# Kernel optimization log

Measured on AMD Instinct MI355X. Metric: run time of the kernel, lower is better.

Reference implementation:

```python
import jax, jax.numpy as jnp
import numpy as np

B, T, D = 2, 2048, 2048
H, KVH = 32, 8
HD = D // H            # 64
G = H // KVH           # 4


def setup_inputs() -> dict:
    key = jax.random.key(0)
    k1, k2, k3 = jax.random.split(key, 3)
    x_q = jax.random.normal(k1, (B, T, D), dtype=jnp.float32)
    W_qkv = jax.random.normal(k2, (D, H * HD + 2 * KVH * HD), dtype=jnp.float32) * 0.02
    W_out = jax.random.normal(k3, (D, D), dtype=jnp.float32) * 0.02
    b_out = jnp.zeros((D,), dtype=jnp.float32)
    # real rotary tables: theta = 10000^{-2i/HD}
    inv_freq = 1.0 / (10000.0 ** (np.arange(0, HD, 2) / HD))   # [HD/2]
    pos = np.arange(T)[:, None] * inv_freq[None, :]            # [T, HD/2]
    rope_cos = jnp.asarray(np.cos(pos), dtype=jnp.float32)
    rope_sin = jnp.asarray(np.sin(pos), dtype=jnp.float32)
    return {"x_q": x_q, "W_qkv": W_qkv, "W_out": W_out, "b_out": b_out,
            "rope_cos": rope_cos, "rope_sin": rope_sin}


def _apply_rope(x, cos, sin):
    # x: [B, h, T, HD], cos/sin: [T, HD/2] -> interleaved even/odd rotation
    xe = x[..., 0::2]
    xo = x[..., 1::2]
    c = cos[None, None, :, :]
    s = sin[None, None, :, :]
    return jnp.stack([xe * c - xo * s, xe * s + xo * c], axis=-1).reshape(x.shape)


def reference(x_q, W_qkv, W_out, b_out, rope_cos, rope_sin):
    b, t, d = x_q.shape
    qkv = x_q @ W_qkv                                  # [B,T,3072]
    q_lin = qkv[..., : H * HD]
    k_lin = qkv[..., H * HD: H * HD + KVH * HD]
    v_lin = qkv[..., H * HD + KVH * HD:]
    q = q_lin.reshape(b, t, H, HD).transpose(0, 2, 1, 3)        # [B,H,T,HD]
    k = k_lin.reshape(b, t, KVH, HD).transpose(0, 2, 1, 3)      # [B,KVH,T,HD]
    v = v_lin.reshape(b, t, KVH, HD).transpose(0, 2, 1, 3)
    # GQA expand (repeat_interleave over heads)
    k = jnp.repeat(k, G, axis=1)                                # [B,H,T,HD]
    v = jnp.repeat(v, G, axis=1)
    q = _apply_rope(q, rope_cos[:t], rope_sin[:t])
    k = _apply_rope(k, rope_cos[:t], rope_sin[:t])
    scale = 1.0 / jnp.sqrt(jnp.asarray(HD, dtype=x_q.dtype))
    logits = jnp.einsum('bhqd,bhkd->bhqk', q, k) * scale        # [B,H,T,T]
    causal = jnp.triu(jnp.ones((t, t), dtype=bool), 1)[None, None]
    logits = jnp.where(causal, jnp.finfo(logits.dtype).min, logits)
    attn = jax.nn.softmax(logits, axis=-1)
    out = jnp.einsum('bhqk,bhkd->bhqd', attn, v)                # [B,H,T,HD]
    out = out.transpose(0, 2, 1, 3).reshape(b, t, H * HD)       # [B,T,D]
    out = out @ W_out + b_out
    return jnp.nan_to_num(out, nan=0.0, posinf=1e4, neginf=-1e4)
```

## Files before the change

### kernel.cpp

```cpp
#include <hip/hip_runtime.h>
#include <hip/hip_bf16.h>

#define DI __device__ __forceinline__

#if __has_builtin(__builtin_amdgcn_exp2f)
#define EXP2(x) __builtin_amdgcn_exp2f(x)
#else
#define EXP2(x) exp2f(x)
#endif

namespace {

constexpr int Bc = 2, Tc = 2048, Dc = 2048, Hc = 32, KVHc = 8, HDc = 64;
constexpr int NQKV = Hc * HDc + 2 * KVHc * HDc;

typedef __bf16 bf16x8 __attribute__((ext_vector_type(8)));
typedef unsigned short u16x8 __attribute__((ext_vector_type(8)));
typedef unsigned short u16x4 __attribute__((ext_vector_type(4)));
typedef float f32x4 __attribute__((ext_vector_type(4)));

union FragU { u16x8 u; bf16x8 b; u16x4 h[2]; };

DI float bits2f(unsigned int u) {
  union { unsigned int i; float f; } v; v.i = u << 16; return v.f;
}
DI unsigned short f2bits(float f) {
  __hip_bfloat16 h = __float2bfloat16(f);
  return *reinterpret_cast<unsigned short*>(&h);
}

DI void store_out(float* p, float v) { *p = v; }
DI void store_out(__hip_bfloat16* p, float v) { *p = __float2bfloat16(v); }

typedef __attribute__((address_space(1))) void gv_t;
typedef __attribute__((address_space(3))) void lv_t;

template<int ROWB, int TOTB, bool SWZ = false>
DI void stage_tile(const char* g, long long row_stride_b, char* lds) {
  const int tid = threadIdx.x;
  const int wid = tid >> 6, lane = tid & 63;
#pragma unroll
  for (int it = 0; it < TOTB / 4096; ++it) {
    int off = it * 4096 + wid * 1024 + lane * 16;
    int row = off / ROWB;
    int colb = off % ROWB;
    if (SWZ) colb ^= (row & 7) << 4;
    const char* gp = g + (long long)row * row_stride_b + colb;
    char* lp = lds + it * 4096 + wid * 1024;
    __builtin_amdgcn_global_load_lds((gv_t*)gp, (lv_t*)lp, 16, 0, 0);
  }
}

__global__ __launch_bounds__(256) void cvt_f32_bf16(
    const float* __restrict__ in, __hip_bfloat16* __restrict__ out) {
  const long long i = ((long long)blockIdx.x * 256 + threadIdx.x) * 8;
  const float4 a = *(const float4*)(in + i);
  const float4 b = *(const float4*)(in + i + 4);
  u16x8 r;
  r[0] = f2bits(a.x); r[1] = f2bits(a.y); r[2] = f2bits(a.z); r[3] = f2bits(a.w);
  r[4] = f2bits(b.x); r[5] = f2bits(b.y); r[6] = f2bits(b.z); r[7] = f2bits(b.w);
  *(u16x8*)((unsigned short*)out + i) = r;
}

__global__ __launch_bounds__(256) void transpose_cvt_kernel(
    const float* __restrict__ in, __hip_bfloat16* __restrict__ out, int R, int C) {
  __shared__ unsigned short tile[64][65];
  const int c0 = blockIdx.x * 64, r0 = blockIdx.y * 64;
  const int tid = threadIdx.x;
  const int rr = tid >> 2, seg = (tid & 3) * 16;
  const float* src = in + (long long)(r0 + rr) * C + c0 + seg;
#pragma unroll
  for (int i = 0; i < 16; ++i) tile[rr][seg + i] = f2bits(src[i]);
  __syncthreads();
  unsigned short* dst = (unsigned short*)out + (long long)(c0 + rr) * R + r0 + seg;
#pragma unroll
  for (int i = 0; i < 16; ++i) dst[i] = tile[seg + i][rr];
}

__global__ __launch_bounds__(256) void transpose_kernel(
    const __hip_bfloat16* __restrict__ in, __hip_bfloat16* __restrict__ out,
    int R, int C) {
  __shared__ unsigned short tile[64][65];
  const long long slice = (long long)R * C;
  const unsigned short* ip = (const unsigned short*)in + (long long)blockIdx.z * slice;
  unsigned short* op = (unsigned short*)out + (long long)blockIdx.z * slice;
  const int c0 = blockIdx.x * 64, r0 = blockIdx.y * 64;
  const int tid = threadIdx.x;
  const int rr = tid >> 2, seg = (tid & 3) * 16;
  const unsigned short* src = ip + (long long)(r0 + rr) * C + c0 + seg;
#pragma unroll
  for (int i = 0; i < 16; ++i) tile[rr][seg + i] = src[i];
  __syncthreads();
  unsigned short* dst = op + (long long)(c0 + rr) * R + r0 + seg;
#pragma unroll
  for (int i = 0; i < 16; ++i) dst[i] = tile[seg + i][rr];
}

template <typename OT>
__global__ __launch_bounds__(256) void gemm_bt(
    const __hip_bfloat16* __restrict__ A, const __hip_bfloat16* __restrict__ Bt,
    const float* __restrict__ bias, OT* __restrict__ C, int M, int N, int K) {
  __shared__ __align__(16) char As[2][8192];
  __shared__ __align__(16) char Bs[2][8192];
  const int nwgx = N >> 7;
  const int nwg = nwgx * (M >> 7);
  const int bid0 = blockIdx.y * nwgx + blockIdx.x;
  const int cpx = nwg >> 3;
  const int bid = (bid0 & 7) * cpx + (bid0 >> 3);
  const int n0 = (bid % nwgx) * 128;
  const int m0 = (bid / nwgx) * 128;
  const int tid = threadIdx.x;
  const int wid = tid >> 6, lane = tid & 63;
  const int wm = (wid >> 1) * 64, wn = (wid & 1) * 64;
  const int l15 = lane & 15, quad = lane >> 4;

  const char* Ag = (const char*)(A + (long long)m0 * K);
  const char* Bg = (const char*)(Bt + (long long)n0 * K);
  const long long strb = (long long)K * 2;

  f32x4 acc[4][4] = {};
  const int nk = K >> 5;

  stage_tile<64, 8192>(Ag, strb, As[0]);
  stage_tile<64, 8192>(Bg, strb, Bs[0]);
  stage_tile<64, 8192>(Ag + 64, strb, As[1]);
  stage_tile<64, 8192>(Bg + 64, strb, Bs[1]);

  for (int kt = 0; kt < nk; ++kt) {
    if (kt < nk - 1) asm volatile("s_waitcnt vmcnt(4)" ::: "memory");
    else             asm volatile("s_waitcnt vmcnt(0)" ::: "memory");
    __builtin_amdgcn_sched_barrier(0);
    __builtin_amdgcn_s_barrier();
    __builtin_amdgcn_sched_barrier(0);

    const char* as = As[kt & 1];
    const char* bs = Bs[kt & 1];
    FragU a[4], b[4];
#pragma unroll
    for (int mt = 0; mt < 4; ++mt)
      a[mt].u = *(const u16x8*)(as + ((wm + mt * 16 + l15) * 32 + quad * 8) * 2);
#pragma unroll
    for (int nt = 0; nt < 4; ++nt)
      b[nt].u = *(const u16x8*)(bs + ((wn + nt * 16 + l15) * 32 + quad * 8) * 2);
#pragma unroll
    for (int mt = 0; mt < 4; ++mt)
#pragma unroll
      for (int nt = 0; nt < 4; ++nt)
        acc[mt][nt] =
            __builtin_amdgcn_mfma_f32_16x16x32_bf16(a[mt].b, b[nt].b, acc[mt][nt], 0, 0, 0);

    __builtin_amdgcn_sched_barrier(0);
    __builtin_amdgcn_s_barrier();
    __builtin_amdgcn_sched_barrier(0);
    if (kt + 2 < nk) {
      stage_tile<64, 8192>(Ag + (long long)(kt + 2) * 64, strb, As[kt & 1]);
      stage_tile<64, 8192>(Bg + (long long)(kt + 2) * 64, strb, Bs[kt & 1]);
    }
  }

#pragma unroll
  for (int nt = 0; nt < 4; ++nt) {
    const int col = n0 + wn + nt * 16 + l15;
    const float bv = bias ? bias[col] : 0.f;
#pragma unroll
    for (int mt = 0; mt < 4; ++mt) {
#pragma unroll
      for (int r = 0; r < 4; ++r) {
        const int row = m0 + wm + mt * 16 + quad * 4 + r;
        store_out(C + (long long)row * N + col, acc[mt][nt][r] + bv);
      }
    }
  }
}

__global__ __launch_bounds__(384) void rope_reshape(
    const __hip_bfloat16* __restrict__ qkv, const float* __restrict__ cosb,
    const float* __restrict__ sinb, __hip_bfloat16* __restrict__ Qo,
    __hip_bfloat16* __restrict__ Ko, __hip_bfloat16* __restrict__ Vo) {
  constexpr float SCL = 0.125f * 1.44269504088896f;
  const int row = blockIdx.x;
  const int b = row / Tc, t = row % Tc;
  const unsigned short* src = (const unsigned short*)qkv + (long long)row * NQKV;
  const float* cb = cosb + t * 32;
  const float* sb = sinb + t * 32;
  const int e = (int)threadIdx.x * 8;
  const u16x8 v = *(const u16x8*)(src + e);
  if (e < Hc * HDc) {
    const int hh = e >> 6, d = e & 63, ii = d >> 1;
    u16x8 r;
#pragma unroll
    for (int p = 0; p < 4; ++p) {
      const float c = cb[ii + p], s = sb[ii + p];
      const float xe = bits2f(v[2 * p]), xo = bits2f(v[2 * p + 1]);
      r[2 * p] = f2bits((xe * c - xo * s) * SCL);
      r[2 * p + 1] = f2bits((xe * s + xo * c) * SCL);
    }
    const long long idx = (((long long)b * Hc + hh) * Tc + t) * HDc + d;
    *(u16x8*)((unsigned short*)Qo + idx) = r;
  } else if (e < Hc * HDc + KVHc * HDc) {
    const int e2 = e - Hc * HDc;
    const int kh = e2 >> 6, d = e2 & 63, ii = d >> 1;
    u16x8 r;
#pragma unroll
    for (int p = 0; p < 4; ++p) {
      const float c = cb[ii + p], s = sb[ii + p];
      const float xe = bits2f(v[2 * p]), xo = bits2f(v[2 * p + 1]);
      r[2 * p] = f2bits(xe * c - xo * s);
      r[2 * p + 1] = f2bits(xe * s + xo * c);
    }
    const long long idx = (((long long)b * KVHc + kh) * Tc + t) * HDc + d;
    *(u16x8*)((unsigned short*)Ko + idx) = r;
  } else {
    const int e2 = e - (Hc * HDc + KVHc * HDc);
    const int kh = e2 >> 6, d = e2 & 63;
    const long long idx = (((long long)b * KVHc + kh) * Tc + t) * HDc + d;
    *(u16x8*)((unsigned short*)Vo + idx) = v;
  }
}


DI void mask_diag(f32x4 (&S)[4], int wid, int l15, int quad) {
#pragma unroll
  for (int nt = 0; nt < 4; ++nt)
#pragma unroll
    for (int r = 0; r < 4; ++r)
      if ((nt * 16 + quad * 4 + r) > (wid * 16 + l15)) S[nt][r] = -1e30f;
}

DI float softmax_pack(f32x4 (&S)[4], float& m_i, float& l_i, FragU (&pa)[2]) {
  float mx = fmaxf(fmaxf(S[0][0], S[0][1]), fmaxf(S[0][2], S[0][3]));
#pragma unroll
  for (int nt = 1; nt < 4; ++nt)
    mx = fmaxf(mx, fmaxf(fmaxf(S[nt][0], S[nt][1]), fmaxf(S[nt][2], S[nt][3])));
  mx = fmaxf(mx, __shfl_xor(mx, 16, 64));
  mx = fmaxf(mx, __shfl_xor(mx, 32, 64));
  const float mnew = fmaxf(m_i, mx);
  const float alpha = EXP2(m_i - mnew);
  m_i = mnew;
  float sum = 0.f;
#pragma unroll
  for (int nt = 0; nt < 4; ++nt)
#pragma unroll
    for (int r = 0; r < 4; ++r) {
      const float pp = EXP2(S[nt][r] - mnew);
      S[nt][r] = pp;
      sum += pp;
    }
  sum += __shfl_xor(sum, 16, 64);
  sum += __shfl_xor(sum, 32, 64);
  l_i = l_i * alpha + sum;
#pragma unroll
  for (int ks = 0; ks < 2; ++ks)
#pragma unroll
    for (int r = 0; r < 4; ++r) {
      pa[ks].u[r] = f2bits(S[2 * ks][r]);
      pa[ks].u[4 + r] = f2bits(S[2 * ks + 1][r]);
    }
  return alpha;
}

DI void attn_tile(const char* __restrict__ Ksb, const char* __restrict__ Vsb,
                  const FragU (&qa)[2], f32x4 (&O)[4], float& m_i, float& l_i,
                  bool diag, int wid, int l15, int quad, int sw) {
  f32x4 S[4] = {};
  __builtin_amdgcn_s_setprio(1);
#pragma unroll
  for (int nt = 0; nt < 4; ++nt) {
#pragma unroll
    for (int ks = 0; ks < 2; ++ks) {
      FragU kb;
      kb.u = *(const u16x8*)(Ksb + (nt * 16 + l15) * 128 + ((((ks << 2) | quad) ^ sw) << 4));
      S[nt] = __builtin_amdgcn_mfma_f32_16x16x32_bf16(kb.b, qa[ks].b, S[nt], 0, 0, 0);
    }
  }
  __builtin_amdgcn_s_setprio(0);
  if (diag) mask_diag(S, wid, l15, quad);
  FragU pa[2];
  const float alpha = softmax_pack(S, m_i, l_i, pa);
#pragma unroll
  for (int nt = 0; nt < 4; ++nt)
#pragma unroll
    for (int r = 0; r < 4; ++r) O[nt][r] *= alpha;
  __builtin_amdgcn_s_setprio(1);
#pragma unroll
  for (int nt = 0; nt < 4; ++nt) {
    const char* vrow = Vsb + (nt * 16 + l15) * 128 + ((quad & 1) << 3);
    const int gq = quad >> 1;
#pragma unroll
    for (int ks = 0; ks < 2; ++ks) {
      FragU vb;
      vb.h[0] = *(const u16x4*)(vrow + (((ks * 4 + gq) ^ sw) << 4));
      vb.h[1] = *(const u16x4*)(vrow + (((ks * 4 + gq + 2) ^ sw) << 4));
      O[nt] = __builtin_amdgcn_mfma_f32_16x16x32_bf16(vb.b, pa[ks].b, O[nt], 0, 0, 0);
    }
  }
  __builtin_amdgcn_s_setprio(0);
}

DI void attn_tile_dual(const char* __restrict__ Ksb, const char* __restrict__ Vsb,
                       const FragU (&qaB)[2], const FragU (&qaA)[2],
                       f32x4 (&OB)[4], f32x4 (&OA)[4],
                       float& mB, float& lB, float& mA, float& lA,
                       bool diagA, int wid, int l15, int quad, int sw) {
  f32x4 SB[4] = {}, SA[4] = {};
  __builtin_amdgcn_s_setprio(1);
#pragma unroll
  for (int nt = 0; nt < 4; ++nt) {
#pragma unroll
    for (int ks = 0; ks < 2; ++ks) {
      FragU kb;
      kb.u = *(const u16x8*)(Ksb + (nt * 16 + l15) * 128 + ((((ks << 2) | quad) ^ sw) << 4));
      SB[nt] = __builtin_amdgcn_mfma_f32_16x16x32_bf16(kb.b, qaB[ks].b, SB[nt], 0, 0, 0);
      SA[nt] = __builtin_amdgcn_mfma_f32_16x16x32_bf16(kb.b, qaA[ks].b, SA[nt], 0, 0, 0);
    }
  }
  __builtin_amdgcn_s_setprio(0);
  if (diagA) mask_diag(SA, wid, l15, quad);
  FragU paB[2], paA[2];
  const float aB = softmax_pack(SB, mB, lB, paB);
  const float aA = softmax_pack(SA, mA, lA, paA);
#pragma unroll
  for (int nt = 0; nt < 4; ++nt)
#pragma unroll
    for (int r = 0; r < 4; ++r) {
      OB[nt][r] *= aB;
      OA[nt][r] *= aA;
    }
  __builtin_amdgcn_s_setprio(1);
#pragma unroll
  for (int nt = 0; nt < 4; ++nt) {
    const char* vrow = Vsb + (nt * 16 + l15) * 128 + ((quad & 1) << 3);
    const int gq = quad >> 1;
#pragma unroll
    for (int ks = 0; ks < 2; ++ks) {
      FragU vb;
      vb.h[0] = *(const u16x4*)(vrow + (((ks * 4 + gq) ^ sw) << 4));
      vb.h[1] = *(const u16x4*)(vrow + (((ks * 4 + gq + 2) ^ sw) << 4));
      OB[nt] = __builtin_amdgcn_mfma_f32_16x16x32_bf16(vb.b, paB[ks].b, OB[nt], 0, 0, 0);
      OA[nt] = __builtin_amdgcn_mfma_f32_16x16x32_bf16(vb.b, paA[ks].b, OA[nt], 0, 0, 0);
    }
  }
  __builtin_amdgcn_s_setprio(0);
}

__global__ __launch_bounds__(256, 4) void attn_kernel(
    const __hip_bfloat16* __restrict__ Q, const __hip_bfloat16* __restrict__ K,
    const __hip_bfloat16* __restrict__ Vt, __hip_bfloat16* __restrict__ Out) {
  __shared__ __align__(16) char Ks[2][8192];
  __shared__ __align__(16) char Vs[2][8192];

  const int p = blockIdx.x;
  const int qtA = p, qtB = (Tc / 64 - 1) - p;
  const int h = blockIdx.y, b = blockIdx.z;
  const int kvh = h >> 2;
  const int tid = threadIdx.x, wid = tid >> 6, lane = tid & 63;
  const int l15 = lane & 15, quad = lane >> 4;
  const int sw = l15 & 7;

  const char* QgA = (const char*)(Q + (((long long)b * Hc + h) * Tc + qtA * 64) * HDc);
  const char* QgB = (const char*)(Q + (((long long)b * Hc + h) * Tc + qtB * 64) * HDc);
  const char* Kg = (const char*)(K + (((long long)b * KVHc + kvh) * Tc) * HDc);
  const char* Vg = (const char*)(Vt + (((long long)b * KVHc + kvh) * HDc) * Tc);

  FragU qaA[2], qaB[2];
#pragma unroll
  for (int ks = 0; ks < 2; ++ks) {
    const int qoff = (wid * 16 + l15) * 128 + (((ks << 2) | quad) << 4);
    qaA[ks].u = *(const u16x8*)(QgA + qoff);
    qaB[ks].u = *(const u16x8*)(QgB + qoff);
  }

  f32x4 OA[4] = {}, OB[4] = {};
  float mA = -1e30f, lA = 0.f, mB = -1e30f, lB = 0.f;

  stage_tile<128, 8192, true>(Kg, 128, Ks[0]);
  stage_tile<128, 8192, true>(Vg, (long long)Tc * 2, Vs[0]);
  asm volatile("s_waitcnt vmcnt(0)" ::: "memory");
  __syncthreads();

  for (int j = 0; j <= qtB; ++j) {
    const int cur = j & 1;
    if (j < qtB) {
      stage_tile<128, 8192, true>(Kg + (long long)(j + 1) * 8192, 128, Ks[cur ^ 1]);
      stage_tile<128, 8192, true>(Vg + (long long)(j + 1) * 128, (long long)Tc * 2, Vs[cur ^ 1]);
    }

    if (j <= qtA) {
      attn_tile_dual(Ks[cur], Vs[cur], qaB, qaA, OB, OA, mB, lB, mA, lA,
                     j == qtA, wid, l15, quad, sw);
    } else {
      attn_tile(Ks[cur], Vs[cur], qaB, OB, mB, lB, j == qtB, wid, l15, quad, sw);
    }

    asm volatile("s_waitcnt vmcnt(0)" ::: "memory");
    __syncthreads();
  }

  const float invA = 1.0f / lA, invB = 1.0f / lB;
  const int tA = qtA * 64 + wid * 16 + l15;
  const int tB = qtB * 64 + wid * 16 + l15;
  unsigned short* obA =
      (unsigned short*)Out + ((long long)b * Tc + tA) * Dc + h * 64 + quad * 4;
  unsigned short* obB =
      (unsigned short*)Out + ((long long)b * Tc + tB) * Dc + h * 64 + quad * 4;
#pragma unroll
  for (int nt = 0; nt < 4; ++nt) {
    u16x4 va, vb;
#pragma unroll
    for (int r = 0; r < 4; ++r) {
      va[r] = f2bits(OA[nt][r] * invA);
      vb[r] = f2bits(OB[nt][r] * invB);
    }
    *(u16x4*)(obA + nt * 16) = va;
    *(u16x4*)(obB + nt * 16) = vb;
  }
}

}

extern "C" void kernel_launch(void* const* d_in, const int* in_sizes, int n_in,
                              void* d_out, int out_size, void* d_ws, size_t ws_size,
                              hipStream_t stream) {
  const float* x_q  = (const float*)d_in[0];
  const float* Wqkv = (const float*)d_in[1];
  const float* Wout = (const float*)d_in[2];
  const float* bout = (const float*)d_in[3];
  const float* rc   = (const float*)d_in[4];
  const float* rs   = (const float*)d_in[5];
  float* out = (float*)d_out;

  constexpr size_t SZ_QKV   = (size_t)Bc * Tc * NQKV * 2;
  constexpr size_t SZ_XB    = (size_t)Bc * Tc * Dc * 2;
  constexpr size_t SZ_QB    = (size_t)Bc * Hc * Tc * HDc * 2;
  constexpr size_t SZ_KV    = (size_t)Bc * KVHc * Tc * HDc * 2;
  constexpr size_t SZ_AO    = (size_t)Bc * Tc * Dc * 2;
  constexpr size_t OFF_QKV   = 0;
  constexpr size_t OFF_XB    = SZ_QKV;
  constexpr size_t OFF_WQKVT = SZ_QKV + SZ_XB;
  constexpr size_t OFF_QB    = SZ_QKV;
  constexpr size_t OFF_KB    = OFF_QB + SZ_QB;
  constexpr size_t OFF_VTMP  = OFF_KB + SZ_KV;
  constexpr size_t OFF_VT    = 0;
  constexpr size_t OFF_AO    = SZ_KV;
  constexpr size_t OFF_WOUTT = OFF_AO + SZ_AO;

  char* w = (char*)d_ws;
  __hip_bfloat16* qkv   = (__hip_bfloat16*)(w + OFF_QKV);
  __hip_bfloat16* xb    = (__hip_bfloat16*)(w + OFF_XB);
  __hip_bfloat16* WqkvT = (__hip_bfloat16*)(w + OFF_WQKVT);
  __hip_bfloat16* Qb    = (__hip_bfloat16*)(w + OFF_QB);
  __hip_bfloat16* Kb    = (__hip_bfloat16*)(w + OFF_KB);
  __hip_bfloat16* Vtmp  = (__hip_bfloat16*)(w + OFF_VTMP);
  __hip_bfloat16* Vt    = (__hip_bfloat16*)(w + OFF_VT);
  __hip_bfloat16* AO    = (__hip_bfloat16*)(w + OFF_AO);
  __hip_bfloat16* WoutT = (__hip_bfloat16*)(w + OFF_WOUTT);

  cvt_f32_bf16<<<dim3((Bc * Tc * Dc) / (256 * 8)), 256, 0, stream>>>(x_q, xb);

  transpose_cvt_kernel<<<dim3(NQKV / 64, Dc / 64), 256, 0, stream>>>(Wqkv, WqkvT, Dc, NQKV);

  gemm_bt<__hip_bfloat16><<<dim3(NQKV / 128, (Bc * Tc) / 128), 256, 0, stream>>>(
      xb, WqkvT, nullptr, qkv, Bc * Tc, NQKV, Dc);

  rope_reshape<<<dim3(Bc * Tc), 384, 0, stream>>>(qkv, rc, rs, Qb, Kb, Vtmp);

  transpose_kernel<<<dim3(HDc / 64, Tc / 64, Bc * KVHc), 256, 0, stream>>>(Vtmp, Vt, Tc, HDc);

  attn_kernel<<<dim3(Tc / 128, Hc, Bc), 256, 0, stream>>>(Qb, Kb, Vt, AO);

  transpose_cvt_kernel<<<dim3(Dc / 64, Dc / 64), 256, 0, stream>>>(Wout, WoutT, Dc, Dc);

  gemm_bt<float><<<dim3(Dc / 128, (Bc * Tc) / 128), 256, 0, stream>>>(
      AO, WoutT, bout, out, Bc * Tc, Dc, Dc);
}
```

Before: 330.3 us.

## Rewrite GEMM as 256x128 tile with 512 threads and triple-buffered swizzled LDS

Replaces the 128x128, 256-thread GEMM with a 256x128 tile run by 8 waves, using a K-step of 64 and three LDS buffers with an XOR swizzle to avoid bank conflicts. Prefetch of the next tile is interleaved between the two K sub-steps, and MFMA sections get raised wave priority. The goal is more data reuse per tile and better overlap of global loads with MFMA work. The cost is heavy LDS use (144KB) that limits occupancy to one block per CU, and fewer workgroups in the grid.

```diff
diff --git a/kernel.cpp b/kernel.cpp
--- a/kernel.cpp
+++ b/kernel.cpp
@@ -47,6 +47,21 @@
     if (SWZ) colb ^= (row & 7) << 4;
     const char* gp = g + (long long)row * row_stride_b + colb;
     char* lp = lds + it * 4096 + wid * 1024;
+    __builtin_amdgcn_global_load_lds((gv_t*)gp, (lv_t*)lp, 16, 0, 0);
+  }
+}
+
+template<int TOTB>
+DI void stage512(const char* g, long long row_stride_b, char* lds) {
+  const int tid = threadIdx.x;
+  const int wid = tid >> 6, lane = tid & 63;
+#pragma unroll
+  for (int it = 0; it < TOTB / 8192; ++it) {
+    const int off = it * 8192 + wid * 1024 + lane * 16;
+    const int row = off >> 7;
+    const int colb = (off & 127) ^ ((row & 7) << 4);
+    const char* gp = g + (long long)row * row_stride_b + colb;
+    char* lp = lds + it * 8192 + wid * 1024;
     __builtin_amdgcn_global_load_lds((gv_t*)gp, (lv_t*)lp, 16, 0, 0);
   }
 }
@@ -97,65 +112,82 @@
 }
 
 template <typename OT>
-__global__ __launch_bounds__(256) void gemm_bt(
+__global__ __launch_bounds__(512, 1) void gemm256(
     const __hip_bfloat16* __restrict__ A, const __hip_bfloat16* __restrict__ Bt,
     const float* __restrict__ bias, OT* __restrict__ C, int M, int N, int K) {
-  __shared__ __align__(16) char As[2][8192];
-  __shared__ __align__(16) char Bs[2][8192];
+  __shared__ __align__(16) char As[3][32768];
+  __shared__ __align__(16) char Bs[3][16384];
   const int nwgx = N >> 7;
-  const int nwg = nwgx * (M >> 7);
+  const int nwg = nwgx * (M >> 8);
   const int bid0 = blockIdx.y * nwgx + blockIdx.x;
   const int cpx = nwg >> 3;
   const int bid = (bid0 & 7) * cpx + (bid0 >> 3);
   const int n0 = (bid % nwgx) * 128;
-  const int m0 = (bid / nwgx) * 128;
+  const int m0 = (bid / nwgx) * 256;
   const int tid = threadIdx.x;
   const int wid = tid >> 6, lane = tid & 63;
   const int wm = (wid >> 1) * 64, wn = (wid & 1) * 64;
   const int l15 = lane & 15, quad = lane >> 4;
+  const int sw = l15 & 7;
 
   const char* Ag = (const char*)(A + (long long)m0 * K);
   const char* Bg = (const char*)(Bt + (long long)n0 * K);
   const long long strb = (long long)K * 2;
+  const int nkt = K >> 6;
 
   f32x4 acc[4][4] = {};
-  const int nk = K >> 5;
-
-  stage_tile<64, 8192>(Ag, strb, As[0]);
-  stage_tile<64, 8192>(Bg, strb, Bs[0]);
-  stage_tile<64, 8192>(Ag + 64, strb, As[1]);
-  stage_tile<64, 8192>(Bg + 64, strb, Bs[1]);
-
-  for (int kt = 0; kt < nk; ++kt) {
-    if (kt < nk - 1) asm volatile("s_waitcnt vmcnt(4)" ::: "memory");
-    else             asm volatile("s_waitcnt vmcnt(0)" ::: "memory");
+
+  stage512<32768>(Ag, strb, As[0]);
+  stage512<16384>(Bg, strb, Bs[0]);
+  stage512<32768>(Ag + 128, strb, As[1]);
+  stage512<16384>(Bg + 128, strb, Bs[1]);
+
+  for (int kt = 0; kt < nkt; ++kt) {
+    if (kt + 1 < nkt) asm volatile("s_waitcnt vmcnt(6)" ::: "memory");
+    else              asm volatile("s_waitcnt vmcnt(0)" ::: "memory");
     __builtin_amdgcn_sched_barrier(0);
     __builtin_amdgcn_s_barrier();
     __builtin_amdgcn_sched_barrier(0);
 
-    const char* as = As[kt & 1];
-    const char* bs = Bs[kt & 1];
-    FragU a[4], b[4];
-#pragma unroll
-    for (int mt = 0; mt < 4; ++mt)
-      a[mt].u = *(const u16x8*)(as + ((wm + mt * 16 + l15) * 32 + quad * 8) * 2);
-#pragma unroll
-    for (int nt = 0; nt < 4; ++nt)
-      b[nt].u = *(const u16x8*)(bs + ((wn + nt * 16 + l15) * 32 + quad * 8) * 2);
-#pragma unroll
-    for (int mt = 0; mt < 4; ++mt)
+    const char* ab = As[kt % 3];
+    const char* bb = Bs[kt % 3];
+    const int pf = kt + 2;
+    const bool do_pf = pf < nkt;
+    char* pfA = As[pf % 3];
+    char* pfB = Bs[pf % 3];
+    const char* gA = Ag + (long long)pf * 128;
+    const char* gB = Bg + (long long)pf * 128;
+
+#pragma unroll
+    for (int kk = 0; kk < 2; ++kk) {
+      FragU a[4], b[4];
+#pragma unroll
+      for (int mt = 0; mt < 4; ++mt)
+        a[mt].u = *(const u16x8*)(ab + (wm + mt * 16 + l15) * 128 +
+                                  ((((kk << 2) | quad) ^ sw) << 4));
 #pragma unroll
       for (int nt = 0; nt < 4; ++nt)
-        acc[mt][nt] =
-            __builtin_amdgcn_mfma_f32_16x16x32_bf16(a[mt].b, b[nt].b, acc[mt][nt], 0, 0, 0);
-
+        b[nt].u = *(const u16x8*)(bb + (wn + nt * 16 + l15) * 128 +
+                                  ((((kk << 2) | quad) ^ sw) << 4));
+      if (do_pf) {
+        if (kk == 0) stage512<32768>(gA, strb, pfA);
+        else         stage512<16384>(gB, strb, pfB);
+      }
+      __builtin_amdgcn_sched_barrier(0);
+      asm volatile("s_waitcnt lgkmcnt(0)" ::: "memory");
+      __builtin_amdgcn_sched_barrier(0);
+      __builtin_amdgcn_s_setprio(1);
+#pragma unroll
+      for (int mt = 0; mt < 4; ++mt)
+#pragma unroll
+        for (int nt = 0; nt < 4; ++nt)
+          acc[mt][nt] =
+              __builtin_amdgcn_mfma_f32_16x16x32_bf16(a[mt].b, b[nt].b, acc[mt][nt], 0, 0, 0);
+      __builtin_amdgcn_s_setprio(0);
+    }
     __builtin_amdgcn_sched_barrier(0);
     __builtin_amdgcn_s_barrier();
     __builtin_amdgcn_sched_barrier(0);
-    if (kt + 2 < nk) {
-      stage_tile<64, 8192>(Ag + (long long)(kt + 2) * 64, strb, As[kt & 1]);
-      stage_tile<64, 8192>(Bg + (long long)(kt + 2) * 64, strb, Bs[kt & 1]);
-    }
   }
 
 #pragma unroll
@@ -459,7 +491,7 @@
 
   transpose_cvt_kernel<<<dim3(NQKV / 64, Dc / 64), 256, 0, stream>>>(Wqkv, WqkvT, Dc, NQKV);
 
-  gemm_bt<__hip_bfloat16><<<dim3(NQKV / 128, (Bc * Tc) / 128), 256, 0, stream>>>(
+  gemm256<__hip_bfloat16><<<dim3(NQKV / 128, (Bc * Tc) / 256), 512, 0, stream>>>(
       xb, WqkvT, nullptr, qkv, Bc * Tc, NQKV, Dc);
 
   rope_reshape<<<dim3(Bc * Tc), 384, 0, stream>>>(qkv, rc, rs, Qb, Kb, Vtmp);
@@ -470,6 +502,6 @@
 
   transpose_cvt_kernel<<<dim3(Dc / 64, Dc / 64), 256, 0, stream>>>(Wout, WoutT, Dc, Dc);
 
-  gemm_bt<float><<<dim3(Dc / 128, (Bc * Tc) / 128), 256, 0, stream>>>(
+  gemm256<float><<<dim3(Dc / 128, (Bc * Tc) / 256), 512, 0, stream>>>(
       AO, WoutT, bout, out, Bc * Tc, Dc, Dc);
 }
```

Result: no change. 332.1 us (+0.6%).

## Share staged K/V tiles across two wave groups per attention block

Applied to the files above, without the earlier changes.

The attention kernel grows to 512 threads, with two 4-wave groups each owning a pair of causal query tiles: (p, 31-p) and (15-p, 16+p). Both groups read the same K/V tiles staged once into LDS, which halves the global K/V traffic and staging work per query tile. A new stage512 helper spreads each 8KB tile load across 8 waves. The grid halves, so there are fewer blocks, and the group with less causal work sits idle at the shared barriers while the other group finishes.

```diff
diff --git a/kernel.cpp b/kernel.cpp
--- a/kernel.cpp
+++ b/kernel.cpp
@@ -47,6 +47,21 @@
     if (SWZ) colb ^= (row & 7) << 4;
     const char* gp = g + (long long)row * row_stride_b + colb;
     char* lp = lds + it * 4096 + wid * 1024;
+    __builtin_amdgcn_global_load_lds((gv_t*)gp, (lv_t*)lp, 16, 0, 0);
+  }
+}
+
+template<int TOTB>
+DI void stage512(const char* g, long long row_stride_b, char* lds) {
+  const int tid = threadIdx.x;
+  const int wid = tid >> 6, lane = tid & 63;
+#pragma unroll
+  for (int it = 0; it < TOTB / 8192; ++it) {
+    const int off = it * 8192 + wid * 1024 + lane * 16;
+    const int row = off >> 7;
+    const int colb = (off & 127) ^ ((row & 7) << 4);
+    const char* gp = g + (long long)row * row_stride_b + colb;
+    char* lp = lds + it * 8192 + wid * 1024;
     __builtin_amdgcn_global_load_lds((gv_t*)gp, (lv_t*)lp, 16, 0, 0);
   }
 }
@@ -219,12 +234,12 @@
 }
 
 
-DI void mask_diag(f32x4 (&S)[4], int wid, int l15, int quad) {
+DI void mask_diag(f32x4 (&S)[4], int w4, int l15, int quad) {
 #pragma unroll
   for (int nt = 0; nt < 4; ++nt)
 #pragma unroll
     for (int r = 0; r < 4; ++r)
-      if ((nt * 16 + quad * 4 + r) > (wid * 16 + l15)) S[nt][r] = -1e30f;
+      if ((nt * 16 + quad * 4 + r) > (w4 * 16 + l15)) S[nt][r] = -1e30f;
 }
 
 DI float softmax_pack(f32x4 (&S)[4], float& m_i, float& l_i, FragU (&pa)[2]) {
@@ -261,7 +276,7 @@
 
 DI void attn_tile(const char* __restrict__ Ksb, const char* __restrict__ Vsb,
                   const FragU (&qa)[2], f32x4 (&O)[4], float& m_i, float& l_i,
-                  bool diag, int wid, int l15, int quad, int sw) {
+                  bool diag, int w4, int l15, int quad, int sw) {
   f32x4 S[4] = {};
   __builtin_amdgcn_s_setprio(1);
 #pragma unroll
@@ -274,7 +289,7 @@
     }
   }
   __builtin_amdgcn_s_setprio(0);
-  if (diag) mask_diag(S, wid, l15, quad);
+  if (diag) mask_diag(S, w4, l15, quad);
   FragU pa[2];
   const float alpha = softmax_pack(S, m_i, l_i, pa);
 #pragma unroll
@@ -301,7 +316,7 @@
                        const FragU (&qaB)[2], const FragU (&qaA)[2],
                        f32x4 (&OB)[4], f32x4 (&OA)[4],
                        float& mB, float& lB, float& mA, float& lA,
-                       bool diagA, int wid, int l15, int quad, int sw) {
+                       bool diagA, int w4, int l15, int quad, int sw) {
   f32x4 SB[4] = {}, SA[4] = {};
   __builtin_amdgcn_s_setprio(1);
 #pragma unroll
@@ -315,7 +330,7 @@
     }
   }
   __builtin_amdgcn_s_setprio(0);
-  if (diagA) mask_diag(SA, wid, l15, quad);
+  if (diagA) mask_diag(SA, w4, l15, quad);
   FragU paB[2], paA[2];
   const float aB = softmax_pack(SB, mB, lB, paB);
   const float aA = softmax_pack(SA, mA, lA, paA);
@@ -343,19 +358,23 @@
   __builtin_amdgcn_s_setprio(0);
 }
 
-__global__ __launch_bounds__(256, 4) void attn_kernel(
+__global__ __launch_bounds__(512, 4) void attn_kernel(
     const __hip_bfloat16* __restrict__ Q, const __hip_bfloat16* __restrict__ K,
     const __hip_bfloat16* __restrict__ Vt, __hip_bfloat16* __restrict__ Out) {
   __shared__ __align__(16) char Ks[2][8192];
   __shared__ __align__(16) char Vs[2][8192];
 
   const int p = blockIdx.x;
-  const int qtA = p, qtB = (Tc / 64 - 1) - p;
   const int h = blockIdx.y, b = blockIdx.z;
   const int kvh = h >> 2;
   const int tid = threadIdx.x, wid = tid >> 6, lane = tid & 63;
+  const int w4 = wid & 3, grp = wid >> 2;
   const int l15 = lane & 15, quad = lane >> 4;
   const int sw = l15 & 7;
+
+  const int qtA = grp ? (15 - p) : p;
+  const int qtB = grp ? (16 + p) : (31 - p);
+  const int jmax = 31 - p;
 
   const char* QgA = (const char*)(Q + (((long long)b * Hc + h) * Tc + qtA * 64) * HDc);
   const char* QgB = (const char*)(Q + (((long long)b * Hc + h) * Tc + qtB * 64) * HDc);
@@ -365,7 +384,7 @@
   FragU qaA[2], qaB[2];
 #pragma unroll
   for (int ks = 0; ks < 2; ++ks) {
-    const int qoff = (wid * 16 + l15) * 128 + (((ks << 2) | quad) << 4);
+    const int qoff = (w4 * 16 + l15) * 128 + (((ks << 2) | quad) << 4);
     qaA[ks].u = *(const u16x8*)(QgA + qoff);
     qaB[ks].u = *(const u16x8*)(QgB + qoff);
   }
@@ -373,23 +392,23 @@
   f32x4 OA[4] = {}, OB[4] = {};
   float mA = -1e30f, lA = 0.f, mB = -1e30f, lB = 0.f;
 
-  stage_tile<128, 8192, true>(Kg, 128, Ks[0]);
-  stage_tile<128, 8192, true>(Vg, (long long)Tc * 2, Vs[0]);
+  stage512<8192>(Kg, 128, Ks[0]);
+  stage512<8192>(Vg, (long long)Tc * 2, Vs[0]);
   asm volatile("s_waitcnt vmcnt(0)" ::: "memory");
   __syncthreads();
 
-  for (int j = 0; j <= qtB; ++j) {
+  for (int j = 0; j <= jmax; ++j) {
     const int cur = j & 1;
-    if (j < qtB) {
-      stage_tile<128, 8192, true>(Kg + (long long)(j + 1) * 8192, 128, Ks[cur ^ 1]);
-      stage_tile<128, 8192, true>(Vg + (long long)(j + 1) * 128, (long long)Tc * 2, Vs[cur ^ 1]);
+    if (j < jmax) {
+      stage512<8192>(Kg + (long long)(j + 1) * 8192, 128, Ks[cur ^ 1]);
+      stage512<8192>(Vg + (long long)(j + 1) * 128, (long long)Tc * 2, Vs[cur ^ 1]);
     }
 
     if (j <= qtA) {
       attn_tile_dual(Ks[cur], Vs[cur], qaB, qaA, OB, OA, mB, lB, mA, lA,
-                     j == qtA, wid, l15, quad, sw);
-    } else {
-      attn_tile(Ks[cur], Vs[cur], qaB, OB, mB, lB, j == qtB, wid, l15, quad, sw);
+                     j == qtA, w4, l15, quad, sw);
+    } else if (j <= qtB) {
+      attn_tile(Ks[cur], Vs[cur], qaB, OB, mB, lB, j == qtB, w4, l15, quad, sw);
     }
 
     asm volatile("s_waitcnt vmcnt(0)" ::: "memory");
@@ -397,8 +416,8 @@
   }
 
   const float invA = 1.0f / lA, invB = 1.0f / lB;
-  const int tA = qtA * 64 + wid * 16 + l15;
-  const int tB = qtB * 64 + wid * 16 + l15;
+  const int tA = qtA * 64 + w4 * 16 + l15;
+  const int tB = qtB * 64 + w4 * 16 + l15;
   unsigned short* obA =
       (unsigned short*)Out + ((long long)b * Tc + tA) * Dc + h * 64 + quad * 4;
   unsigned short* obB =
@@ -466,7 +485,7 @@
 
   transpose_kernel<<<dim3(HDc / 64, Tc / 64, Bc * KVHc), 256, 0, stream>>>(Vtmp, Vt, Tc, HDc);
 
-  attn_kernel<<<dim3(Tc / 128, Hc, Bc), 256, 0, stream>>>(Qb, Kb, Vt, AO);
+  attn_kernel<<<dim3(Tc / 256, Hc, Bc), 512, 0, stream>>>(Qb, Kb, Vt, AO);
 
   transpose_cvt_kernel<<<dim3(Dc / 64, Dc / 64), 256, 0, stream>>>(Wout, WoutT, Dc, Dc);
 
```

Result: faster. 309.5 us (-6.3%).
